# Kernel optimization log

Measured on AMD Instinct MI355X. Metric: run time of the kernel, lower is better.

Reference implementation:

```python
import jax, jax.numpy as jnp
import numpy as np

N_NODES = 100000
N_EDGES = 1600000
IN_FEATS = 128
HIDDEN = 64
OUT_FEATS = 64
N_LABELS = 8


def setup_inputs() -> dict:
    key = jax.random.key(0)
    ks = jax.random.split(key, 10)
    glorot = lambda k, fi, fo: jax.random.normal(k, (fi, fo), jnp.float32) * jnp.sqrt(2.0 / (fi + fo))
    return {
        "features": jax.random.normal(ks[0], (N_NODES, IN_FEATS), jnp.float32),
        "edge_src": jax.random.randint(ks[1], (N_EDGES,), 0, N_NODES, jnp.int32),
        "edge_dst": jax.random.randint(ks[2], (N_EDGES,), 0, N_NODES, jnp.int32),
        "edge_types": jax.random.randint(ks[3], (N_EDGES,), 0, 4, jnp.int32),
        "W1": glorot(ks[4], IN_FEATS, HIDDEN),
        "b1": jnp.zeros((HIDDEN,), jnp.float32),
        "W2": glorot(ks[5], HIDDEN, OUT_FEATS),
        "b2": jnp.zeros((OUT_FEATS,), jnp.float32),
        "Wp": glorot(ks[6], OUT_FEATS, N_LABELS),
        "bp": jnp.zeros((N_LABELS,), jnp.float32),
    }


def _degree_norms(edge_src, edge_dst, n_nodes):
    ones = jnp.ones(edge_src.shape[0], jnp.float32)
    deg_out = jax.ops.segment_sum(ones, edge_src, num_segments=n_nodes)
    deg_in = jax.ops.segment_sum(ones, edge_dst, num_segments=n_nodes)
    # DGL clamps degrees to min 1 before pow(-0.5)
    norm_src = jnp.maximum(deg_out, 1.0) ** -0.5  # [N]
    norm_dst = jnp.maximum(deg_in, 1.0) ** -0.5   # [N]
    return norm_src, norm_dst


def _graph_conv(x, W, b, edge_src, edge_dst, norm_src, norm_dst, n_nodes):
    # norm='both': scale src, dense transform first (mult_first), aggregate, scale dst
    h = (x * norm_src[:, None]) @ W            # [N, out]
    msg = h[edge_src]                          # [E, out] gather
    agg = jax.ops.segment_sum(msg, edge_dst, num_segments=n_nodes)  # [N, out] scatter-add
    return agg * norm_dst[:, None] + b


def reference(features, edge_src, edge_dst, edge_types, W1, b1, W2, b2, Wp, bp):
    n_nodes = features.shape[0]
    norm_src, norm_dst = _degree_norms(edge_src, edge_dst, n_nodes)
    x = jax.nn.relu(_graph_conv(features, W1, b1, edge_src, edge_dst, norm_src, norm_dst, n_nodes))
    # dropout is identity in eval mode
    x = jax.nn.relu(_graph_conv(x, W2, b2, edge_src, edge_dst, norm_src, norm_dst, n_nodes))
    logits = x @ Wp + bp                       # [N, n_labels]
    return jax.nn.softmax(logits, axis=1)
```

## Files before the change

kernel.cpp:

```cpp
#include <hip/hip_runtime.h>
#include <hip/hip_fp16.h>
#include <math.h>


#define NODES   100000
#define INF     128
#define HID     64
#define NLAB    8

#define SB      512
#define NSB     ((NODES + SB - 1) / SB)
#define NHALF   ((NODES + 255) / 256)
#define CAP1    9000
#define SCAP    9000
#define CAP2    4600
#define PCHUNK  4096
#define PEPT    (PCHUNK / 256)
#define SRCMASK 0x1FFFF

#define WCVT_ELEMS (64 * (INF + 8) + 64 * (HID + 8))
#define WCVT_WGS   ((WCVT_ELEMS + 255) / 256)

union H8 { int4 i4; __half2 h2[4]; };

typedef _Float16 half8 __attribute__((ext_vector_type(8)));
typedef float floatx4 __attribute__((ext_vector_type(4)));


__global__ void build1_kernel(const int* __restrict__ src, const int* __restrict__ dst,
                              int* __restrict__ gcur_d, int* __restrict__ gcur_s,
                              int* __restrict__ dreg, unsigned short* __restrict__ sreg,
                              int E, int partWGs,
                              const float* __restrict__ W1, const float* __restrict__ W2,
                              _Float16* __restrict__ wt1, _Float16* __restrict__ wt2) {
    __shared__ int hd[NSB], hs[NSB], bd[NSB], bs[NSB];
    const int tid = threadIdx.x;

    if (blockIdx.x >= partWGs) {
        const int N1 = 64 * (INF + 8);
        const int N2 = 64 * (HID + 8);
        int i = (blockIdx.x - partWGs) * 256 + tid;
        if (i < N1) {
            int n = i / (INF + 8), k = i % (INF + 8);
            wt1[i] = (k < INF) ? (_Float16)W1[k * 64 + n] : (_Float16)0.f;
        } else if (i < N1 + N2) {
            int j = i - N1;
            int n = j / (HID + 8), k = j % (HID + 8);
            wt2[j] = (k < HID) ? (_Float16)W2[k * 64 + n] : (_Float16)0.f;
        }
        return;
    }

    const int e0 = blockIdx.x * PCHUNK;

    for (int i = tid; i < NSB; i += 256) { hd[i] = 0; hs[i] = 0; }
    __syncthreads();

    int es[PEPT], ed[PEPT];
#pragma unroll
    for (int i = 0; i < PEPT; ++i) {
        int e = e0 + tid + i * 256;
        if (e < E) {
            es[i] = src[e]; ed[i] = dst[e];
            atomicAdd(&hd[ed[i] >> 9], 1);
            atomicAdd(&hs[es[i] >> 9], 1);
        } else es[i] = -1;
    }
    __syncthreads();

    for (int b = tid; b < NSB; b += 256) {
        int c = hd[b]; bd[b] = c ? atomicAdd(&gcur_d[b], c) : 0;
        c = hs[b];     bs[b] = c ? atomicAdd(&gcur_s[b], c) : 0;
    }
    __syncthreads();
    for (int b = tid; b < NSB; b += 256) { hd[b] = 0; hs[b] = 0; }
    __syncthreads();

#pragma unroll
    for (int i = 0; i < PEPT; ++i) {
        if (es[i] >= 0) {
            int s = es[i], d = ed[i];
            int kb = d >> 9;
            int pos = bd[kb] + atomicAdd(&hd[kb], 1);
            if (pos < CAP1) dreg[(size_t)kb * CAP1 + pos] = ((d & (SB - 1)) << 17) | s;
            int ks = s >> 9;
            int ps = bs[ks] + atomicAdd(&hs[ks], 1);
            if (ps < SCAP) sreg[(size_t)ks * SCAP + ps] = (unsigned short)(s & (SB - 1));
        }
    }
}


__global__ void shist_kernel(const unsigned short* __restrict__ sreg,
                             const int* __restrict__ gcur_s,
                             float* __restrict__ norm_s, int Nn) {
    __shared__ int hist[SB];
    const int tid = threadIdx.x;
    const int sb = blockIdx.x;
    for (int i = tid; i < SB; i += 256) hist[i] = 0;
    __syncthreads();
    const int cnt = min(gcur_s[sb], SCAP);
    const unsigned short* base = sreg + (size_t)sb * SCAP;
    for (int i = tid; i < cnt; i += 256) atomicAdd(&hist[base[i]], 1);
    __syncthreads();
    for (int t = tid; t < SB; t += 256) {
        int node = sb * SB + t;
        if (node < Nn) norm_s[node] = rsqrtf(fmaxf((float)hist[t], 1.0f));
    }
}


__global__ void build2_kernel(const int* __restrict__ dreg, const int* __restrict__ gcur_d,
                              int* __restrict__ csr, int* __restrict__ starts,
                              int* __restrict__ ends, float* __restrict__ norm_d,
                              const float* __restrict__ Xv, const float* __restrict__ norm,
                              const _Float16* __restrict__ Wt, __half* __restrict__ Hh,
                              int Nn) {
    __shared__ union SMem {
        struct CS { int hist[256]; int excl[256]; int cur[256]; int tot; int sorted[CAP2]; } c;
        _Float16 w[64 * (INF + 8)];
    } sm;
    const int tid = threadIdx.x;

    if (blockIdx.x < NHALF) {
        const int j = blockIdx.x;
        const int sb = j >> 1, half = j & 1;
        const int cnt = min(gcur_d[sb], CAP1);
        const int* reg = dreg + (size_t)sb * CAP1;

        sm.c.hist[tid] = 0;
        __syncthreads();

        for (int i = tid; i < cnt; i += 256) {
            int pe = reg[i];
            if (((pe >> 25) & 1) == half) atomicAdd(&sm.c.hist[(pe >> 17) & 255], 1);
        }
        __syncthreads();

        sm.c.excl[tid] = sm.c.hist[tid];
        __syncthreads();
        for (int off = 1; off < 256; off <<= 1) {
            int v = (tid >= off) ? sm.c.excl[tid - off] : 0;
            __syncthreads();
            sm.c.excl[tid] += v;
            __syncthreads();
        }
        int deg = sm.c.hist[tid];
        int st = sm.c.excl[tid] - deg;
        if (tid == 255) sm.c.tot = min(sm.c.excl[255], CAP2);
        int node = j * 256 + tid;
        if (node < Nn) {
            int gs = j * CAP2 + st;
            int dcl = min(deg, max(CAP2 - st, 0));
            starts[node] = gs;
            ends[node]   = gs + dcl;
            norm_d[node] = rsqrtf(fmaxf((float)deg, 1.0f));
        }
        sm.c.cur[tid] = st;
        __syncthreads();

        for (int i = tid; i < cnt; i += 256) {
            int pe = reg[i];
            if (((pe >> 25) & 1) == half) {
                int pos = atomicAdd(&sm.c.cur[(pe >> 17) & 255], 1);
                if (pos < CAP2) sm.c.sorted[pos] = pe & SRCMASK;
            }
        }
        __syncthreads();

        const int tot = sm.c.tot;
        for (int i = tid; i < tot; i += 256) csr[(size_t)j * CAP2 + i] = sm.c.sorted[i];
        return;
    }

    constexpr int K = INF;
    constexpr int KP = K + 8;
    const int bid = blockIdx.x - NHALF;

    constexpr int NI4 = 64 * KP * 2 / 16;
    for (int i = tid; i < NI4; i += 256)
        ((int4*)sm.w)[i] = ((const int4*)Wt)[i];
    __syncthreads();

    const int w = tid >> 6, lane = tid & 63;
    const int m16 = lane & 15, quad = lane >> 4;
    const int rowA = bid * 64 + w * 16 + m16;
    const int rowC = (rowA < Nn) ? rowA : (Nn - 1);

    floatx4 acc0 = {0.f, 0.f, 0.f, 0.f};
    floatx4 acc1 = acc0, acc2 = acc0, acc3 = acc0;

#pragma unroll
    for (int c = 0; c < K / 32; ++c) {
        const int k0 = c * 32 + quad * 8;
        const float* xrow = Xv + (size_t)rowC * K;
        float4 xa = *(const float4*)(xrow + k0);
        float4 xb = *(const float4*)(xrow + k0 + 4);
        half8 a;
        a[0] = (_Float16)xa.x; a[1] = (_Float16)xa.y;
        a[2] = (_Float16)xa.z; a[3] = (_Float16)xa.w;
        a[4] = (_Float16)xb.x; a[5] = (_Float16)xb.y;
        a[6] = (_Float16)xb.z; a[7] = (_Float16)xb.w;
        half8 b0 = *(const half8*)&sm.w[(0 * 16 + m16) * KP + k0];
        half8 b1 = *(const half8*)&sm.w[(1 * 16 + m16) * KP + k0];
        half8 b2 = *(const half8*)&sm.w[(2 * 16 + m16) * KP + k0];
        half8 b3 = *(const half8*)&sm.w[(3 * 16 + m16) * KP + k0];
        acc0 = __builtin_amdgcn_mfma_f32_16x16x32_f16(a, b0, acc0, 0, 0, 0);
        acc1 = __builtin_amdgcn_mfma_f32_16x16x32_f16(a, b1, acc1, 0, 0, 0);
        acc2 = __builtin_amdgcn_mfma_f32_16x16x32_f16(a, b2, acc2, 0, 0, 0);
        acc3 = __builtin_amdgcn_mfma_f32_16x16x32_f16(a, b3, acc3, 0, 0, 0);
    }

    const int rbase = bid * 64 + w * 16 + quad * 4;
    floatx4 accs[4] = {acc0, acc1, acc2, acc3};
#pragma unroll
    for (int i = 0; i < 4; ++i) {
        int grow = rbase + i;
        if (grow < Nn) {
            float nm = norm[grow];
            __half* o = Hh + (size_t)grow * 64 + m16;
#pragma unroll
            for (int t = 0; t < 4; ++t)
                o[16 * t] = (__half)(accs[t][i] * nm);
        }
    }
}


template <int K, bool IN16>
__global__ void gemm_mfma_kernel(const void* __restrict__ Xv, const float* __restrict__ norm,
                                 const _Float16* __restrict__ Wt, __half* __restrict__ Hh,
                                 int M) {
    constexpr int KP = K + 8;
    __shared__ _Float16 sWt[64 * KP];

    const int tid = threadIdx.x;
    constexpr int NI4 = 64 * KP * 2 / 16;
    for (int i = tid; i < NI4; i += 256)
        ((int4*)sWt)[i] = ((const int4*)Wt)[i];
    __syncthreads();

    const int w = tid >> 6, lane = tid & 63;
    const int m16 = lane & 15, quad = lane >> 4;
    const int rowA = blockIdx.x * 64 + w * 16 + m16;
    const int rowC = (rowA < M) ? rowA : (M - 1);

    floatx4 acc0 = {0.f, 0.f, 0.f, 0.f};
    floatx4 acc1 = acc0, acc2 = acc0, acc3 = acc0;

#pragma unroll
    for (int c = 0; c < K / 32; ++c) {
        const int k0 = c * 32 + quad * 8;
        half8 a;
        if constexpr (IN16) {
            const _Float16* xrow = (const _Float16*)Xv + (size_t)rowC * K;
            a = *(const half8*)(xrow + k0);
        } else {
            const float* xrow = (const float*)Xv + (size_t)rowC * K;
            float4 xa = *(const float4*)(xrow + k0);
            float4 xb = *(const float4*)(xrow + k0 + 4);
            a[0] = (_Float16)xa.x; a[1] = (_Float16)xa.y;
            a[2] = (_Float16)xa.z; a[3] = (_Float16)xa.w;
            a[4] = (_Float16)xb.x; a[5] = (_Float16)xb.y;
            a[6] = (_Float16)xb.z; a[7] = (_Float16)xb.w;
        }
        half8 b0 = *(const half8*)&sWt[(0 * 16 + m16) * KP + k0];
        half8 b1 = *(const half8*)&sWt[(1 * 16 + m16) * KP + k0];
        half8 b2 = *(const half8*)&sWt[(2 * 16 + m16) * KP + k0];
        half8 b3 = *(const half8*)&sWt[(3 * 16 + m16) * KP + k0];
        acc0 = __builtin_amdgcn_mfma_f32_16x16x32_f16(a, b0, acc0, 0, 0, 0);
        acc1 = __builtin_amdgcn_mfma_f32_16x16x32_f16(a, b1, acc1, 0, 0, 0);
        acc2 = __builtin_amdgcn_mfma_f32_16x16x32_f16(a, b2, acc2, 0, 0, 0);
        acc3 = __builtin_amdgcn_mfma_f32_16x16x32_f16(a, b3, acc3, 0, 0, 0);
    }

    const int rbase = blockIdx.x * 64 + w * 16 + quad * 4;
    floatx4 accs[4] = {acc0, acc1, acc2, acc3};
#pragma unroll
    for (int i = 0; i < 4; ++i) {
        int grow = rbase + i;
        if (grow < M) {
            float nm = norm[grow];
            __half* o = Hh + (size_t)grow * 64 + m16;
#pragma unroll
            for (int t = 0; t < 4; ++t)
                o[16 * t] = (__half)(accs[t][i] * nm);
        }
    }
}


__global__ void gather_kernel(const int* __restrict__ starts, const int* __restrict__ ends,
                              const int* __restrict__ csr, const __half* __restrict__ Hh,
                              const float* __restrict__ nd, const float* __restrict__ b,
                              __half* __restrict__ Xh, int Nn) {
    const int tid = threadIdx.x;
    const int lane = tid & 63;
    const int half32 = (lane >> 5) & 1;
    const int l32 = lane & 31;
    const int g = l32 >> 3;
    const int c = lane & 7;

    int node = blockIdx.x * 8 + ((tid >> 6) << 1) + half32;
    const bool valid = node < Nn;
    const int nodeC = valid ? node : (Nn - 1);

    const int start = starts[nodeC];
    const int deg   = ends[nodeC] - start;
    const int dmax  = max(deg, __shfl_xor(deg, 32, 64));

    float acc[8] = {0.f, 0.f, 0.f, 0.f, 0.f, 0.f, 0.f, 0.f};

    for (int base = 0; base < dmax; base += 32) {
        int off = base + l32;
        int pe = (off < deg) ? csr[start + off] : 0;
        int ec  = min(deg - base, 32);
        int ecm = min(dmax - base, 32);
        int nkp = (ecm + 7) >> 3;

        for (int k = 0; k < nkp; ++k) {
            int j0 = g + 8 * k;
            int j1 = j0 + 4;
            int s0 = __shfl(pe, (lane & 32) + j0, 64);
            int s1 = __shfl(pe, (lane & 32) + j1, 64);
            H8 v0, v1;
            if (j0 < ec) v0.i4 = ((const int4*)(Hh + (size_t)s0 * 64))[c];
            else         v0.i4 = make_int4(0, 0, 0, 0);
            if (j1 < ec) v1.i4 = ((const int4*)(Hh + (size_t)s1 * 64))[c];
            else         v1.i4 = make_int4(0, 0, 0, 0);
#pragma unroll
            for (int t = 0; t < 4; ++t) {
                __half2 s = __hadd2(v0.h2[t], v1.h2[t]);
                float2 f = __half22float2(s);
                acc[2 * t]     += f.x;
                acc[2 * t + 1] += f.y;
            }
        }
    }

#pragma unroll
    for (int m = 8; m <= 16; m <<= 1) {
#pragma unroll
        for (int k = 0; k < 8; ++k)
            acc[k] += __shfl_xor(acc[k], m, 64);
    }

    if (g == 0 && valid) {
        float nm = nd[node];
        float4 b0 = ((const float4*)b)[2 * c];
        float4 b1 = ((const float4*)b)[2 * c + 1];
        H8 o;
        o.h2[0] = __floats2half2_rn(fmaxf(fmaf(acc[0], nm, b0.x), 0.f),
                                    fmaxf(fmaf(acc[1], nm, b0.y), 0.f));
        o.h2[1] = __floats2half2_rn(fmaxf(fmaf(acc[2], nm, b0.z), 0.f),
                                    fmaxf(fmaf(acc[3], nm, b0.w), 0.f));
        o.h2[2] = __floats2half2_rn(fmaxf(fmaf(acc[4], nm, b1.x), 0.f),
                                    fmaxf(fmaf(acc[5], nm, b1.y), 0.f));
        o.h2[3] = __floats2half2_rn(fmaxf(fmaf(acc[6], nm, b1.z), 0.f),
                                    fmaxf(fmaf(acc[7], nm, b1.w), 0.f));
        ((int4*)(Xh + (size_t)node * 64))[c] = o.i4;
    }
}


__global__ void proj_softmax_kernel(const __half* __restrict__ Xh, const float* __restrict__ Wp,
                                    const float* __restrict__ bp, float* __restrict__ out, int M) {
    __shared__ float sW[64 * NLAB];
    __shared__ float sb[NLAB];
    int tid = threadIdx.x;
    for (int i = tid; i < 64 * NLAB; i += 256) sW[i] = Wp[i];
    if (tid < NLAB) sb[tid] = bp[tid];
    __syncthreads();

    int row = blockIdx.x * 256 + tid;
    if (row >= M) return;

    float logit[NLAB];
#pragma unroll
    for (int l = 0; l < NLAB; ++l) logit[l] = sb[l];
    const H8* x8 = (const H8*)(Xh + (size_t)row * 64);
#pragma unroll 2
    for (int kk = 0; kk < 8; ++kk) {
        H8 v = x8[kk];
#pragma unroll
        for (int t = 0; t < 4; ++t) {
            float2 f = __half22float2(v.h2[t]);
            int k = kk * 8 + 2 * t;
#pragma unroll
            for (int l = 0; l < NLAB; ++l)
                logit[l] = fmaf(f.x, sW[k * NLAB + l], logit[l]);
#pragma unroll
            for (int l = 0; l < NLAB; ++l)
                logit[l] = fmaf(f.y, sW[(k + 1) * NLAB + l], logit[l]);
        }
    }
    float mx = logit[0];
#pragma unroll
    for (int l = 1; l < NLAB; ++l) mx = fmaxf(mx, logit[l]);
    float s = 0.0f;
#pragma unroll
    for (int l = 0; l < NLAB; ++l) { logit[l] = __expf(logit[l] - mx); s += logit[l]; }
    float inv = 1.0f / s;
#pragma unroll
    for (int l = 0; l < NLAB; ++l) out[(size_t)row * NLAB + l] = logit[l] * inv;
}


extern "C" void kernel_launch(void* const* d_in, const int* in_sizes, int n_in,
                              void* d_out, int out_size, void* d_ws, size_t ws_size,
                              hipStream_t stream) {
    const float* features = (const float*)d_in[0];
    const int*   edge_src = (const int*)d_in[1];
    const int*   edge_dst = (const int*)d_in[2];
    const float* W1 = (const float*)d_in[4];
    const float* b1 = (const float*)d_in[5];
    const float* W2 = (const float*)d_in[6];
    const float* b2 = (const float*)d_in[7];
    const float* Wp = (const float*)d_in[8];
    const float* bp = (const float*)d_in[9];
    float* out = (float*)d_out;

    const int N = NODES;
    const int E = in_sizes[1];

    char* p = (char*)d_ws;
    int*   csr    = (int*)p;            p += sizeof(int) * (size_t)NHALF * CAP2;
    int*   starts = (int*)p;            p += sizeof(int) * N;
    int*   ends   = (int*)p;            p += sizeof(int) * N;
    float* norm_s = (float*)p;          p += sizeof(float) * N;
    float* norm_d = (float*)p;          p += sizeof(float) * N;
    int*   gcur_d = (int*)p;            p += sizeof(int) * NSB;
    int*   gcur_s = (int*)p;            p += sizeof(int) * NSB;
    p = (char*)(((size_t)p + 255) & ~(size_t)255);
    _Float16* wt1 = (_Float16*)p;       p += sizeof(_Float16) * 64 * (INF + 8);
    _Float16* wt2 = (_Float16*)p;       p += sizeof(_Float16) * 64 * (HID + 8);
    p = (char*)(((size_t)p + 255) & ~(size_t)255);
    __half* h     = (__half*)p;         p += sizeof(__half) * (size_t)N * 64;
    p = (char*)(((size_t)p + 255) & ~(size_t)255);
    __half* x     = (__half*)p;         p += sizeof(__half) * (size_t)N * 64;
    int*            dreg = (int*)x;
    unsigned short* sreg = (unsigned short*)((char*)x + sizeof(int) * (size_t)NSB * CAP1);

    hipMemsetAsync(gcur_d, 0, sizeof(int) * 2 * NSB, stream);

    const int partWGs = (E + PCHUNK - 1) / PCHUNK;
    build1_kernel<<<partWGs + WCVT_WGS, 256, 0, stream>>>(edge_src, edge_dst,
                                                          gcur_d, gcur_s, dreg, sreg,
                                                          E, partWGs, W1, W2, wt1, wt2);
    shist_kernel<<<NSB, 256, 0, stream>>>(sreg, gcur_s, norm_s, N);
    build2_kernel<<<NHALF + (N + 63) / 64, 256, 0, stream>>>(dreg, gcur_d, csr, starts,
                                                             ends, norm_d,
                                                             features, norm_s, wt1, h, N);

    gather_kernel<<<(N + 7) / 8, 256, 0, stream>>>(starts, ends, csr, h, norm_d, b1, x, N);

    gemm_mfma_kernel<HID, true><<<(N + 63) / 64, 256, 0, stream>>>(x, norm_s, wt2, h, N);
    gather_kernel<<<(N + 7) / 8, 256, 0, stream>>>(starts, ends, csr, h, norm_d, b2, x, N);

    proj_softmax_kernel<<<(N + 255) / 256, 256, 0, stream>>>(x, Wp, bp, out, N);
}
```

Baseline: 254.1 us.

## Compute source degrees with global atomics and fuse projection-softmax into second gather

```diff
diff --git a/kernel.cpp b/kernel.cpp
--- a/kernel.cpp
+++ b/kernel.cpp
@@ -12,7 +12,6 @@
 #define NSB     ((NODES + SB - 1) / SB)
 #define NHALF   ((NODES + 255) / 256)
 #define CAP1    9000
-#define SCAP    9000
 #define CAP2    4600
 #define PCHUNK  4096
 #define PEPT    (PCHUNK / 256)
@@ -28,12 +27,11 @@
 
 
 __global__ void build1_kernel(const int* __restrict__ src, const int* __restrict__ dst,
-                              int* __restrict__ gcur_d, int* __restrict__ gcur_s,
-                              int* __restrict__ dreg, unsigned short* __restrict__ sreg,
-                              int E, int partWGs,
+                              int* __restrict__ gcur_d, int* __restrict__ deg_s,
+                              int* __restrict__ dreg, int E, int partWGs,
                               const float* __restrict__ W1, const float* __restrict__ W2,
                               _Float16* __restrict__ wt1, _Float16* __restrict__ wt2) {
-    __shared__ int hd[NSB], hs[NSB], bd[NSB], bs[NSB];
+    __shared__ int hd[NSB], bd[NSB];
     const int tid = threadIdx.x;
 
     if (blockIdx.x >= partWGs) {
@@ -53,7 +51,7 @@
 
     const int e0 = blockIdx.x * PCHUNK;
 
-    for (int i = tid; i < NSB; i += 256) { hd[i] = 0; hs[i] = 0; }
+    for (int i = tid; i < NSB; i += 256) hd[i] = 0;
     __syncthreads();
 
     int es[PEPT], ed[PEPT];
@@ -63,17 +61,16 @@
         if (e < E) {
             es[i] = src[e]; ed[i] = dst[e];
             atomicAdd(&hd[ed[i] >> 9], 1);
-            atomicAdd(&hs[es[i] >> 9], 1);
+            atomicAdd(&deg_s[es[i]], 1);
         } else es[i] = -1;
     }
     __syncthreads();
 
     for (int b = tid; b < NSB; b += 256) {
         int c = hd[b]; bd[b] = c ? atomicAdd(&gcur_d[b], c) : 0;
-        c = hs[b];     bs[b] = c ? atomicAdd(&gcur_s[b], c) : 0;
-    }
-    __syncthreads();
-    for (int b = tid; b < NSB; b += 256) { hd[b] = 0; hs[b] = 0; }
+    }
+    __syncthreads();
+    for (int b = tid; b < NSB; b += 256) hd[b] = 0;
     __syncthreads();
 
 #pragma unroll
@@ -83,29 +80,7 @@
             int kb = d >> 9;
             int pos = bd[kb] + atomicAdd(&hd[kb], 1);
             if (pos < CAP1) dreg[(size_t)kb * CAP1 + pos] = ((d & (SB - 1)) << 17) | s;
-            int ks = s >> 9;
-            int ps = bs[ks] + atomicAdd(&hs[ks], 1);
-            if (ps < SCAP) sreg[(size_t)ks * SCAP + ps] = (unsigned short)(s & (SB - 1));
-        }
-    }
-}
-
-
-__global__ void shist_kernel(const unsigned short* __restrict__ sreg,
-                             const int* __restrict__ gcur_s,
-                             float* __restrict__ norm_s, int Nn) {
-    __shared__ int hist[SB];
-    const int tid = threadIdx.x;
-    const int sb = blockIdx.x;
-    for (int i = tid; i < SB; i += 256) hist[i] = 0;
-    __syncthreads();
-    const int cnt = min(gcur_s[sb], SCAP);
-    const unsigned short* base = sreg + (size_t)sb * SCAP;
-    for (int i = tid; i < cnt; i += 256) atomicAdd(&hist[base[i]], 1);
-    __syncthreads();
-    for (int t = tid; t < SB; t += 256) {
-        int node = sb * SB + t;
-        if (node < Nn) norm_s[node] = rsqrtf(fmaxf((float)hist[t], 1.0f));
+        }
     }
 }
 
@@ -113,7 +88,7 @@
 __global__ void build2_kernel(const int* __restrict__ dreg, const int* __restrict__ gcur_d,
                               int* __restrict__ csr, int* __restrict__ starts,
                               int* __restrict__ ends, float* __restrict__ norm_d,
-                              const float* __restrict__ Xv, const float* __restrict__ norm,
+                              const float* __restrict__ Xv, const int* __restrict__ deg,
                               const _Float16* __restrict__ Wt, __half* __restrict__ Hh,
                               int Nn) {
     __shared__ union SMem {
@@ -145,16 +120,16 @@
             sm.c.excl[tid] += v;
             __syncthreads();
         }
-        int deg = sm.c.hist[tid];
-        int st = sm.c.excl[tid] - deg;
+        int deg_n = sm.c.hist[tid];
+        int st = sm.c.excl[tid] - deg_n;
         if (tid == 255) sm.c.tot = min(sm.c.excl[255], CAP2);
         int node = j * 256 + tid;
         if (node < Nn) {
             int gs = j * CAP2 + st;
-            int dcl = min(deg, max(CAP2 - st, 0));
+            int dcl = min(deg_n, max(CAP2 - st, 0));
             starts[node] = gs;
             ends[node]   = gs + dcl;
-            norm_d[node] = rsqrtf(fmaxf((float)deg, 1.0f));
+            norm_d[node] = rsqrtf(fmaxf((float)deg_n, 1.0f));
         }
         sm.c.cur[tid] = st;
         __syncthreads();
@@ -217,7 +192,7 @@
     for (int i = 0; i < 4; ++i) {
         int grow = rbase + i;
         if (grow < Nn) {
-            float nm = norm[grow];
+            float nm = rsqrtf(fmaxf((float)deg[grow], 1.0f));
             __half* o = Hh + (size_t)grow * 64 + m16;
 #pragma unroll
             for (int t = 0; t < 4; ++t)
@@ -228,7 +203,7 @@
 
 
 template <int K, bool IN16>
-__global__ void gemm_mfma_kernel(const void* __restrict__ Xv, const float* __restrict__ norm,
+__global__ void gemm_mfma_kernel(const void* __restrict__ Xv, const int* __restrict__ deg,
                                  const _Float16* __restrict__ Wt, __half* __restrict__ Hh,
                                  int M) {
     constexpr int KP = K + 8;
@@ -280,7 +255,7 @@
     for (int i = 0; i < 4; ++i) {
         int grow = rbase + i;
         if (grow < M) {
-            float nm = norm[grow];
+            float nm = rsqrtf(fmaxf((float)deg[grow], 1.0f));
             __half* o = Hh + (size_t)grow * 64 + m16;
 #pragma unroll
             for (int t = 0; t < 4; ++t)
@@ -290,11 +265,26 @@
 }
 
 
+template <bool PROJ>
 __global__ void gather_kernel(const int* __restrict__ starts, const int* __restrict__ ends,
                               const int* __restrict__ csr, const __half* __restrict__ Hh,
                               const float* __restrict__ nd, const float* __restrict__ b,
-                              __half* __restrict__ Xh, int Nn) {
+                              __half* __restrict__ Xh, const float* __restrict__ Wp,
+                              const float* __restrict__ bp, float* __restrict__ out,
+                              int Nn) {
+    __shared__ float sW[NLAB * 65];
+    __shared__ float sb_[NLAB];
     const int tid = threadIdx.x;
+
+    if constexpr (PROJ) {
+        for (int i = tid; i < 64 * NLAB; i += 256) {
+            int k = i >> 3, l = i & 7;
+            sW[l * 65 + k] = Wp[i];
+        }
+        if (tid < NLAB) sb_[tid] = bp[tid];
+        __syncthreads();
+    }
+
     const int lane = tid & 63;
     const int half32 = (lane >> 5) & 1;
     const int l32 = lane & 31;
@@ -345,64 +335,61 @@
             acc[k] += __shfl_xor(acc[k], m, 64);
     }
 
-    if (g == 0 && valid) {
-        float nm = nd[node];
+    if constexpr (!PROJ) {
+        if (g == 0 && valid) {
+            float nm = nd[node];
+            float4 b0 = ((const float4*)b)[2 * c];
+            float4 b1 = ((const float4*)b)[2 * c + 1];
+            H8 o;
+            o.h2[0] = __floats2half2_rn(fmaxf(fmaf(acc[0], nm, b0.x), 0.f),
+                                        fmaxf(fmaf(acc[1], nm, b0.y), 0.f));
+            o.h2[1] = __floats2half2_rn(fmaxf(fmaf(acc[2], nm, b0.z), 0.f),
+                                        fmaxf(fmaf(acc[3], nm, b0.w), 0.f));
+            o.h2[2] = __floats2half2_rn(fmaxf(fmaf(acc[4], nm, b1.x), 0.f),
+                                        fmaxf(fmaf(acc[5], nm, b1.y), 0.f));
+            o.h2[3] = __floats2half2_rn(fmaxf(fmaf(acc[6], nm, b1.z), 0.f),
+                                        fmaxf(fmaf(acc[7], nm, b1.w), 0.f));
+            ((int4*)(Xh + (size_t)node * 64))[c] = o.i4;
+        }
+    } else {
+        float nm = nd[nodeC];
         float4 b0 = ((const float4*)b)[2 * c];
         float4 b1 = ((const float4*)b)[2 * c + 1];
-        H8 o;
-        o.h2[0] = __floats2half2_rn(fmaxf(fmaf(acc[0], nm, b0.x), 0.f),
-                                    fmaxf(fmaf(acc[1], nm, b0.y), 0.f));
-        o.h2[1] = __floats2half2_rn(fmaxf(fmaf(acc[2], nm, b0.z), 0.f),
-                                    fmaxf(fmaf(acc[3], nm, b0.w), 0.f));
-        o.h2[2] = __floats2half2_rn(fmaxf(fmaf(acc[4], nm, b1.x), 0.f),
-                                    fmaxf(fmaf(acc[5], nm, b1.y), 0.f));
-        o.h2[3] = __floats2half2_rn(fmaxf(fmaf(acc[6], nm, b1.z), 0.f),
-                                    fmaxf(fmaf(acc[7], nm, b1.w), 0.f));
-        ((int4*)(Xh + (size_t)node * 64))[c] = o.i4;
-    }
-}
-
-
-__global__ void proj_softmax_kernel(const __half* __restrict__ Xh, const float* __restrict__ Wp,
-                                    const float* __restrict__ bp, float* __restrict__ out, int M) {
-    __shared__ float sW[64 * NLAB];
-    __shared__ float sb[NLAB];
-    int tid = threadIdx.x;
-    for (int i = tid; i < 64 * NLAB; i += 256) sW[i] = Wp[i];
-    if (tid < NLAB) sb[tid] = bp[tid];
-    __syncthreads();
-
-    int row = blockIdx.x * 256 + tid;
-    if (row >= M) return;
-
-    float logit[NLAB];
-#pragma unroll
-    for (int l = 0; l < NLAB; ++l) logit[l] = sb[l];
-    const H8* x8 = (const H8*)(Xh + (size_t)row * 64);
-#pragma unroll 2
-    for (int kk = 0; kk < 8; ++kk) {
-        H8 v = x8[kk];
-#pragma unroll
-        for (int t = 0; t < 4; ++t) {
-            float2 f = __half22float2(v.h2[t]);
-            int k = kk * 8 + 2 * t;
-#pragma unroll
-            for (int l = 0; l < NLAB; ++l)
-                logit[l] = fmaf(f.x, sW[k * NLAB + l], logit[l]);
-#pragma unroll
-            for (int l = 0; l < NLAB; ++l)
-                logit[l] = fmaf(f.y, sW[(k + 1) * NLAB + l], logit[l]);
-        }
-    }
-    float mx = logit[0];
-#pragma unroll
-    for (int l = 1; l < NLAB; ++l) mx = fmaxf(mx, logit[l]);
-    float s = 0.0f;
-#pragma unroll
-    for (int l = 0; l < NLAB; ++l) { logit[l] = __expf(logit[l] - mx); s += logit[l]; }
-    float inv = 1.0f / s;
-#pragma unroll
-    for (int l = 0; l < NLAB; ++l) out[(size_t)row * NLAB + l] = logit[l] * inv;
+        float xv[8];
+        xv[0] = fmaxf(fmaf(acc[0], nm, b0.x), 0.f);
+        xv[1] = fmaxf(fmaf(acc[1], nm, b0.y), 0.f);
+        xv[2] = fmaxf(fmaf(acc[2], nm, b0.z), 0.f);
+        xv[3] = fmaxf(fmaf(acc[3], nm, b0.w), 0.f);
+        xv[4] = fmaxf(fmaf(acc[4], nm, b1.x), 0.f);
+        xv[5] = fmaxf(fmaf(acc[5], nm, b1.y), 0.f);
+        xv[6] = fmaxf(fmaf(acc[6], nm, b1.z), 0.f);
+        xv[7] = fmaxf(fmaf(acc[7], nm, b1.w), 0.f);
+
+        const int l0 = 2 * g, l1 = l0 + 1;
+        float p0 = 0.f, p1 = 0.f;
+#pragma unroll
+        for (int j = 0; j < 8; ++j) {
+            p0 = fmaf(xv[j], sW[l0 * 65 + 8 * c + j], p0);
+            p1 = fmaf(xv[j], sW[l1 * 65 + 8 * c + j], p1);
+        }
+        p0 += __shfl_xor(p0, 1, 64); p1 += __shfl_xor(p1, 1, 64);
+        p0 += __shfl_xor(p0, 2, 64); p1 += __shfl_xor(p1, 2, 64);
+        p0 += __shfl_xor(p0, 4, 64); p1 += __shfl_xor(p1, 4, 64);
+        p0 += sb_[l0];
+        p1 += sb_[l1];
+        float mx = fmaxf(p0, p1);
+        mx = fmaxf(mx, __shfl_xor(mx, 8, 64));
+        mx = fmaxf(mx, __shfl_xor(mx, 16, 64));
+        float e0 = __expf(p0 - mx), e1 = __expf(p1 - mx);
+        float s2 = e0 + e1;
+        s2 += __shfl_xor(s2, 8, 64);
+        s2 += __shfl_xor(s2, 16, 64);
+        float inv = 1.0f / s2;
+        if (c == 0 && valid) {
+            float2 o = {e0 * inv, e1 * inv};
+            *(float2*)(out + (size_t)node * NLAB + l0) = o;
+        }
+    }
 }
 
 
@@ -427,10 +414,9 @@
     int*   csr    = (int*)p;            p += sizeof(int) * (size_t)NHALF * CAP2;
     int*   starts = (int*)p;            p += sizeof(int) * N;
     int*   ends   = (int*)p;            p += sizeof(int) * N;
-    float* norm_s = (float*)p;          p += sizeof(float) * N;
     float* norm_d = (float*)p;          p += sizeof(float) * N;
     int*   gcur_d = (int*)p;            p += sizeof(int) * NSB;
-    int*   gcur_s = (int*)p;            p += sizeof(int) * NSB;
+    int*   deg_s  = (int*)p;            p += sizeof(int) * N;
     p = (char*)(((size_t)p + 255) & ~(size_t)255);
     _Float16* wt1 = (_Float16*)p;       p += sizeof(_Float16) * 64 * (INF + 8);
     _Float16* wt2 = (_Float16*)p;       p += sizeof(_Float16) * 64 * (HID + 8);
@@ -438,24 +424,23 @@
     __half* h     = (__half*)p;         p += sizeof(__half) * (size_t)N * 64;
     p = (char*)(((size_t)p + 255) & ~(size_t)255);
     __half* x     = (__half*)p;         p += sizeof(__half) * (size_t)N * 64;
-    int*            dreg = (int*)x;
-    unsigned short* sreg = (unsigned short*)((char*)x + sizeof(int) * (size_t)NSB * CAP1);
-
-    hipMemsetAsync(gcur_d, 0, sizeof(int) * 2 * NSB, stream);
+    int* dreg = (int*)x;
+
+    hipMemsetAsync(gcur_d, 0, sizeof(int) * (NSB + N), stream);
 
     const int partWGs = (E + PCHUNK - 1) / PCHUNK;
     build1_kernel<<<partWGs + WCVT_WGS, 256, 0, stream>>>(edge_src, edge_dst,
-                                                          gcur_d, gcur_s, dreg, sreg,
+                                                          gcur_d, deg_s, dreg,
                                                           E, partWGs, W1, W2, wt1, wt2);
-    shist_kernel<<<NSB, 256, 0, stream>>>(sreg, gcur_s, norm_s, N);
     build2_kernel<<<NHALF + (N + 63) / 64, 256, 0, stream>>>(dreg, gcur_d, csr, starts,
                                                              ends, norm_d,
-                                                             features, norm_s, wt1, h, N);
-
-    gather_kernel<<<(N + 7) / 8, 256, 0, stream>>>(starts, ends, csr, h, norm_d, b1, x, N);
-
-    gemm_mfma_kernel<HID, true><<<(N + 63) / 64, 256, 0, stream>>>(x, norm_s, wt2, h, N);
-    gather_kernel<<<(N + 7) / 8, 256, 0, stream>>>(starts, ends, csr, h, norm_d, b2, x, N);
-
-    proj_softmax_kernel<<<(N + 255) / 256, 256, 0, stream>>>(x, Wp, bp, out, N);
+                                                             features, deg_s, wt1, h, N);
+
+    gather_kernel<false><<<(N + 7) / 8, 256, 0, stream>>>(starts, ends, csr, h, norm_d,
+                                                          b1, x, nullptr, nullptr,
+                                                          nullptr, N);
+
+    gemm_mfma_kernel<HID, true><<<(N + 63) / 64, 256, 0, stream>>>(x, deg_s, wt2, h, N);
+    gather_kernel<true><<<(N + 7) / 8, 256, 0, stream>>>(starts, ends, csr, h, norm_d,
+                                                         b2, nullptr, Wp, bp, out, N);
 }
```

Result: slower. 284.2 us (+11.9%).
